# Performance work log

Measured on AMD Instinct MI355X. Metric: run time of the kernel, lower is better.

The kernel has to match this reference:

```python
import jax, jax.numpy as jnp
import numpy as np
from math import sqrt

B, L, S, H, E, D = 4, 2048, 2048, 16, 64, 64


def setup_inputs() -> dict:
    key = jax.random.key(0)
    kq, kk, kv = jax.random.split(key, 3)
    queries = jax.random.normal(kq, (B, L, H, E), dtype=jnp.float32)
    keys = jax.random.normal(kk, (B, S, H, E), dtype=jnp.float32)
    values = jax.random.normal(kv, (B, S, H, D), dtype=jnp.float32)
    # TriangularCausalMask: True above the diagonal (positions to mask out)
    attn_mask = jnp.broadcast_to(
        jnp.triu(jnp.ones((L, S), dtype=bool), k=1)[None, None], (B, 1, L, S)
    )
    return {"queries": queries, "keys": keys, "values": values, "attn_mask": attn_mask}


def reference(queries, keys, values, attn_mask):
    # B, L, H, E = queries.shape ; scale = 1/sqrt(E) (self.scale is None)
    scale = 1.0 / sqrt(queries.shape[-1])
    # scores: [B, H, L, S]
    scores = jnp.einsum("blhe,bshe->bhls", queries, keys)
    # mask_flag=True: masked_fill with -inf before scaling (scale*(-inf) = -inf)
    scores = jnp.where(attn_mask, -jnp.inf, scores)
    A = jax.nn.softmax(scale * scores, axis=-1)  # dropout p=0.0 -> identity
    V = jnp.einsum("bhls,bshd->blhd", A, values)
    return V
```

## Files before the change

### kernel.cpp

```cpp
#include <hip/hip_runtime.h>
#include <hip/hip_bf16.h>

typedef __bf16 bf16x8 __attribute__((ext_vector_type(8)));
typedef float floatx4 __attribute__((ext_vector_type(4)));
typedef unsigned int u32;

#define Bc 4
#define Lc 2048
#define Sc 2048
#define Hc 16
#define Ec 64
#define Dc 64
#define NQT (Lc/64)
#define NPAIR (NQT/2)
#define NT (Sc/64)
#define TILEB 8192
#define WSK ((size_t)Bc*Hc*NT*TILEB)
#define WSNEED (2*WSK)

__device__ __forceinline__ bf16x8 pack8f(const float* f){
  bf16x8 r;
  #pragma unroll
  for (int i=0;i<8;++i) r[i] = (__bf16)f[i];
  return r;
}

template<int CTRL>
__device__ __forceinline__ float dppf(float x){
  return __builtin_bit_cast(float,
    __builtin_amdgcn_update_dpp(0, __builtin_bit_cast(int, x), CTRL, 0xF, 0xF, true));
}
__device__ __forceinline__ float rowmax16(float x){
  x = fmaxf(x, dppf<0xB1>(x));
  x = fmaxf(x, dppf<0x4E>(x));
  x = fmaxf(x, dppf<0x141>(x));
  x = fmaxf(x, dppf<0x140>(x));
  return x;
}
__device__ __forceinline__ float rowsum16(float x){
  x += dppf<0xB1>(x);
  x += dppf<0x4E>(x);
  x += dppf<0x141>(x);
  x += dppf<0x140>(x);
  return x;
}

__device__ __forceinline__ void gload16(const void* g, void* l){
  __builtin_amdgcn_global_load_lds(
      (const __attribute__((address_space(1))) u32*)g,
      (__attribute__((address_space(3))) u32*)l, 16, 0, 0);
}

__global__ __launch_bounds__(256)
void prep(const float* __restrict__ K, const float* __restrict__ V,
          char* __restrict__ ws)
{
  const int t = blockIdx.x*256 + threadIdx.x;
  if (t < (1<<20)) {
    const int c = t & 7, r = (t>>3) & 63, tile = (t>>9) & 31, h = (t>>14) & 15, b = t>>18;
    const float* src = K + ((size_t)((b*Sc + tile*64 + r))*Hc + h)*Ec + c*8;
    float tmp[8];
    *(float4*)(tmp)   = *(const float4*)(src);
    *(float4*)(tmp+4) = *(const float4*)(src + 4);
    char* dst = ws + (size_t)((b*Hc + h)*NT + tile)*TILEB + r*128 + ((c ^ (r&7))<<4);
    *(bf16x8*)dst = pack8f(tmp);
  } else {
    const int u = t - (1<<20);
    const int d = u & 63, c = (u>>6) & 7, tile = (u>>9) & 31, h = (u>>14) & 15, b = u>>18;
    const float* src = V + ((size_t)((b*Sc + tile*64 + c*8))*Hc + h)*Dc + d;
    bf16x8 v;
    #pragma unroll
    for (int kk=0; kk<8; ++kk) v[kk] = (__bf16)src[(size_t)kk*Hc*Dc];
    char* dst = ws + WSK + (size_t)((b*Hc + h)*NT + tile)*TILEB + d*128 + ((c ^ (d&7))<<4);
    *(bf16x8*)dst = v;
  }
}

__global__ __launch_bounds__(256)
void fa_fwd(const float* __restrict__ Q, const char* __restrict__ ws,
            float* __restrict__ O)
{
  int nid = blockIdx.x;
  int bid = (nid & 7) * ((int)gridDim.x >> 3) + (nid >> 3);
  int pid = bid & (NPAIR - 1);
  int h  = (bid >> 4) & (Hc - 1);
  int b  = bid >> 8;

  int tid  = threadIdx.x;
  int w    = tid >> 6;
  int lane = tid & 63;
  int lg   = lane >> 4;
  int lr   = lane & 15;

  __shared__ __align__(16) char Kl[2][64*128];
  __shared__ __align__(16) char Vl[2][64*128];
  __shared__ __align__(16) char Pl[4][16*64*2];
  char* Pw = Pl[w];

  const char* gK = ws +        (size_t)((b*Hc + h)*NT)*TILEB;
  const char* gV = ws + WSK +  (size_t)((b*Hc + h)*NT)*TILEB;
  const int soff = w*2048 + lane*16;

  #pragma unroll 1
  for (int pass=0; pass<2; ++pass) {
    const int qt = pass ? (NQT-1-pid) : pid;

    const int qrow = qt*64 + w*16 + lr;
    const float* qp = Q + ((size_t)(b*Lc + qrow)*Hc + h)*Ec;
    bf16x8 aq[2];
    {
      float tmp[8];
      #pragma unroll
      for (int c=0; c<2; ++c) {
        *(float4*)(tmp)   = *(const float4*)(qp + c*32 + lg*8);
        *(float4*)(tmp+4) = *(const float4*)(qp + c*32 + lg*8 + 4);
        #pragma unroll
        for (int i=0;i<8;++i) tmp[i] *= 0.125f;
        aq[c] = pack8f(tmp);
      }
    }

    floatx4 o[4];
    float m[4], lsum[4];
    #pragma unroll
    for (int i=0;i<4;++i){ o[i] = (floatx4){0.f,0.f,0.f,0.f}; m[i] = -3.0e38f; lsum[i] = 0.f; }

    {
      const char* sK = gK + soff;
      const char* sV = gV + soff;
      gload16(sK,        &Kl[0][w*2048]);
      gload16(sK + 1024, &Kl[0][w*2048 + 1024]);
      gload16(sV,        &Vl[0][w*2048]);
      gload16(sV + 1024, &Vl[0][w*2048 + 1024]);
    }
    __syncthreads();

    const int nt = qt + 1;
    for (int t = 0; t < nt; ++t) {
      char* Kcur = Kl[t&1];
      char* Vcur = Vl[t&1];

      if (t+1 < nt) {
        const int nb = (t+1)&1;
        const char* sK = gK + (size_t)(t+1)*TILEB + soff;
        const char* sV = gV + (size_t)(t+1)*TILEB + soff;
        gload16(sK,        &Kl[nb][w*2048]);
        gload16(sK + 1024, &Kl[nb][w*2048 + 1024]);
        gload16(sV,        &Vl[nb][w*2048]);
        gload16(sV + 1024, &Vl[nb][w*2048 + 1024]);
      }

      floatx4 s[4];
      #pragma unroll
      for (int nf=0; nf<4; ++nf) {
        int kr = nf*16 + lr;
        unsigned xr = (kr & 7) << 4;
        const char* kp = Kcur + kr*128;
        bf16x8 b0 = *(const bf16x8*)(kp + ((lg*16)      ^ xr));
        bf16x8 b1 = *(const bf16x8*)(kp + ((64 + lg*16) ^ xr));
        floatx4 acc = (floatx4){0.f,0.f,0.f,0.f};
        acc = __builtin_amdgcn_mfma_f32_16x16x32_bf16(aq[0], b0, acc, 0, 0, 0);
        acc = __builtin_amdgcn_mfma_f32_16x16x32_bf16(aq[1], b1, acc, 0, 0, 0);
        s[nf] = acc;
      }

      if (t == qt) {
        #pragma unroll
        for (int nf=0; nf<4; ++nf)
          #pragma unroll
          for (int r=0; r<4; ++r)
            if (nf*16 + lr > w*16 + lg*4 + r) s[nf][r] = -3.0e38f;
      }

      float mx[4], rs[4], al[4];
      #pragma unroll
      for (int r=0;r<4;++r) {
        mx[r] = rowmax16(fmaxf(fmaxf(s[0][r], s[1][r]), fmaxf(s[2][r], s[3][r])));
        float mn = fmaxf(m[r], mx[r]);
        al[r] = __expf(m[r] - mn);
        m[r] = mn;
        rs[r] = 0.f;
      }
      #pragma unroll
      for (int nf=0; nf<4; ++nf)
        #pragma unroll
        for (int r=0;r<4;++r) {
          float p = __expf(s[nf][r] - m[r]);
          rs[r] += p;
          s[nf][r] = p;
        }
      #pragma unroll
      for (int r=0;r<4;++r) {
        rs[r] = rowsum16(rs[r]);
        lsum[r] = lsum[r]*al[r] + rs[r];
      }
      #pragma unroll
      for (int df=0; df<4; ++df)
        #pragma unroll
        for (int r=0;r<4;++r) o[df][r] *= al[r];

      #pragma unroll
      for (int nf=0; nf<4; ++nf)
        #pragma unroll
        for (int r=0;r<4;++r) {
          int q = lg*4 + r;
          int k = nf*16 + lr;
          *(__bf16*)(Pw + q*128 + ((k*2) ^ ((q&7)<<4))) = (__bf16)s[nf][r];
        }

      {
        unsigned xq = (lr & 7) << 4;
        const char* pp = Pw + lr*128;
        bf16x8 pa0 = *(const bf16x8*)(pp + ((lg*16)      ^ xq));
        bf16x8 pa1 = *(const bf16x8*)(pp + ((64 + lg*16) ^ xq));
        #pragma unroll
        for (int df=0; df<4; ++df) {
          int d = df*16 + lr;
          unsigned xd = (d & 7) << 4;
          const char* vp = Vcur + d*128;
          bf16x8 vb0 = *(const bf16x8*)(vp + ((lg*16)      ^ xd));
          bf16x8 vb1 = *(const bf16x8*)(vp + ((64 + lg*16) ^ xd));
          o[df] = __builtin_amdgcn_mfma_f32_16x16x32_bf16(pa0, vb0, o[df], 0, 0, 0);
          o[df] = __builtin_amdgcn_mfma_f32_16x16x32_bf16(pa1, vb1, o[df], 0, 0, 0);
        }
      }
      __syncthreads();
    }

    #pragma unroll
    for (int r=0;r<4;++r) {
      float inv = 1.0f / lsum[r];
      int qg = qt*64 + w*16 + lg*4 + r;
      float* op = O + ((size_t)(b*Lc + qg)*Hc + h)*Dc;
      #pragma unroll
      for (int df=0; df<4; ++df)
        op[df*16 + lr] = o[df][r] * inv;
    }
  }
}

#define QB 128
#define NQTB (Lc/QB)
#define NPAIRB (NQTB/2)

__global__ __launch_bounds__(256)
void fa_fwd_fb(const float* __restrict__ Q, const float* __restrict__ K,
               const float* __restrict__ V, float* __restrict__ O)
{
  int nid = blockIdx.x;
  int bid = (nid & 7) * ((int)gridDim.x >> 3) + (nid >> 3);
  int pid = bid & (NPAIRB - 1);
  int h  = (bid >> 3) & (Hc - 1);
  int b  = bid >> 7;

  int tid  = threadIdx.x;
  int w    = tid >> 6;
  int lane = tid & 63;
  int lg   = lane >> 4;
  int lr   = lane & 15;

  __shared__ __align__(16) char Kl[2][64*128];
  __shared__ __align__(16) char Vl[2][64*128];
  __shared__ __align__(16) char Pl[4][16*64*2];
  char* Pw = Pl[w];

  const int skr = tid >> 2, seg = tid & 3;
  const int sd  = tid & 63, skb = tid >> 6;
  const unsigned xk = (skr & 7) << 4;
  const unsigned xv = (sd  & 7) << 4;

  const float* Kb = K + ((size_t)(b*Sc)*Hc + h)*Ec;
  const float* Vb = V + ((size_t)(b*Sc)*Hc + h)*Dc;

  float kf[16], vf[16];

  #pragma unroll 1
  for (int pass=0; pass<2; ++pass) {
    const int qtb = pass ? (NQTB-1-pid) : pid;
    const int q0w = qtb*QB + w*32;

    bf16x8 aq[2][2];
    #pragma unroll
    for (int s2=0; s2<2; ++s2) {
      const float* qp = Q + ((size_t)(b*Lc + q0w + s2*16 + lr)*Hc + h)*Ec;
      float tmp[8];
      #pragma unroll
      for (int c=0; c<2; ++c) {
        *(float4*)(tmp)   = *(const float4*)(qp + c*32 + lg*8);
        *(float4*)(tmp+4) = *(const float4*)(qp + c*32 + lg*8 + 4);
        #pragma unroll
        for (int i=0;i<8;++i) tmp[i] *= 0.125f;
        aq[s2][c] = pack8f(tmp);
      }
    }

    floatx4 o[2][4];
    float m[2][4], lsum[2][4];
    #pragma unroll
    for (int s2=0; s2<2; ++s2)
      #pragma unroll
      for (int i=0;i<4;++i){ o[s2][i] = (floatx4){0.f,0.f,0.f,0.f}; m[s2][i] = -3.0e38f; lsum[s2][i] = 0.f; }

    {
      const float* ks = Kb + (size_t)skr*Hc*Ec + seg*16;
      *(float4*)(kf)    = *(const float4*)(ks);
      *(float4*)(kf+4)  = *(const float4*)(ks+4);
      *(float4*)(kf+8)  = *(const float4*)(ks+8);
      *(float4*)(kf+12) = *(const float4*)(ks+12);
      const float* vs = Vb + (size_t)(skb*16)*Hc*Dc + sd;
      #pragma unroll
      for (int i=0;i<16;++i) vf[i] = vs[(size_t)i*Hc*Dc];
    }

    const int nt = 2*qtb + 2;
    for (int t = 0; t < nt; ++t) {
      char* Kcur = Kl[t&1];
      char* Vcur = Vl[t&1];

      *(bf16x8*)(Kcur + skr*128 + ((seg*32)      ^ xk)) = pack8f(kf);
      *(bf16x8*)(Kcur + skr*128 + ((seg*32 + 16) ^ xk)) = pack8f(kf+8);
      *(bf16x8*)(Vcur + sd*128  + ((skb*32)      ^ xv)) = pack8f(vf);
      *(bf16x8*)(Vcur + sd*128  + ((skb*32 + 16) ^ xv)) = pack8f(vf+8);
      __syncthreads();

      if (t+1 < nt) {
        const float* ks = Kb + (size_t)((t+1)*64 + skr)*Hc*Ec + seg*16;
        *(float4*)(kf)    = *(const float4*)(ks);
        *(float4*)(kf+4)  = *(const float4*)(ks+4);
        *(float4*)(kf+8)  = *(const float4*)(ks+8);
        *(float4*)(kf+12) = *(const float4*)(ks+12);
        const float* vs = Vb + (size_t)((t+1)*64 + skb*16)*Hc*Dc + sd;
        #pragma unroll
        for (int i=0;i<16;++i) vf[i] = vs[(size_t)i*Hc*Dc];
      }

      if (t*64 <= q0w + 31) {
        const int t64 = t*64;
        const bool needmask = (t64 + 63 > q0w);

        #pragma unroll
        for (int s2=0; s2<2; ++s2) {
          floatx4 s[4];
          #pragma unroll
          for (int nf=0; nf<4; ++nf) {
            int kr = nf*16 + lr;
            unsigned xr = (kr & 7) << 4;
            const char* kp = Kcur + kr*128;
            bf16x8 b0 = *(const bf16x8*)(kp + ((lg*16)      ^ xr));
            bf16x8 b1 = *(const bf16x8*)(kp + ((64 + lg*16) ^ xr));
            floatx4 acc = (floatx4){0.f,0.f,0.f,0.f};
            acc = __builtin_amdgcn_mfma_f32_16x16x32_bf16(aq[s2][0], b0, acc, 0, 0, 0);
            acc = __builtin_amdgcn_mfma_f32_16x16x32_bf16(aq[s2][1], b1, acc, 0, 0, 0);
            s[nf] = acc;
          }

          if (needmask) {
            const int qq = q0w + s2*16 + lg*4;
            #pragma unroll
            for (int nf=0; nf<4; ++nf)
              #pragma unroll
              for (int r=0; r<4; ++r)
                if (t64 + nf*16 + lr > qq + r) s[nf][r] = -3.0e38f;
          }

          float mx[4], rs[4], al[4];
          #pragma unroll
          for (int r=0;r<4;++r) {
            mx[r] = rowmax16(fmaxf(fmaxf(s[0][r], s[1][r]), fmaxf(s[2][r], s[3][r])));
            float mn = fmaxf(m[s2][r], mx[r]);
            al[r] = __expf(m[s2][r] - mn);
            m[s2][r] = mn;
            rs[r] = 0.f;
          }
          #pragma unroll
          for (int nf=0; nf<4; ++nf)
            #pragma unroll
            for (int r=0;r<4;++r) {
              float p = __expf(s[nf][r] - m[s2][r]);
              rs[r] += p;
              s[nf][r] = p;
            }
          #pragma unroll
          for (int r=0;r<4;++r) {
            rs[r] = rowsum16(rs[r]);
            lsum[s2][r] = lsum[s2][r]*al[r] + rs[r];
          }
          #pragma unroll
          for (int df=0; df<4; ++df)
            #pragma unroll
            for (int r=0;r<4;++r) o[s2][df][r] *= al[r];

          #pragma unroll
          for (int nf=0; nf<4; ++nf)
            #pragma unroll
            for (int r=0;r<4;++r) {
              int q = lg*4 + r;
              int k = nf*16 + lr;
              *(__bf16*)(Pw + q*128 + ((k*2) ^ ((q&7)<<4))) = (__bf16)s[nf][r];
            }

          {
            unsigned xq = (lr & 7) << 4;
            const char* pp = Pw + lr*128;
            bf16x8 pa0 = *(const bf16x8*)(pp + ((lg*16)      ^ xq));
            bf16x8 pa1 = *(const bf16x8*)(pp + ((64 + lg*16) ^ xq));
            #pragma unroll
            for (int df=0; df<4; ++df) {
              int d = df*16 + lr;
              unsigned xd = (d & 7) << 4;
              const char* vp = Vcur + d*128;
              bf16x8 vb0 = *(const bf16x8*)(vp + ((lg*16)      ^ xd));
              bf16x8 vb1 = *(const bf16x8*)(vp + ((64 + lg*16) ^ xd));
              o[s2][df] = __builtin_amdgcn_mfma_f32_16x16x32_bf16(pa0, vb0, o[s2][df], 0, 0, 0);
              o[s2][df] = __builtin_amdgcn_mfma_f32_16x16x32_bf16(pa1, vb1, o[s2][df], 0, 0, 0);
            }
          }
        }
      }
      __syncthreads();
    }

    #pragma unroll
    for (int s2=0; s2<2; ++s2)
      #pragma unroll
      for (int r=0;r<4;++r) {
        float inv = 1.0f / lsum[s2][r];
        int qg = q0w + s2*16 + lg*4 + r;
        float* op = O + ((size_t)(b*Lc + qg)*Hc + h)*Dc;
        #pragma unroll
        for (int df=0; df<4; ++df)
          op[df*16 + lr] = o[s2][df][r] * inv;
      }
  }
}

extern "C" void kernel_launch(void* const* d_in, const int* in_sizes, int n_in,
                              void* d_out, int out_size, void* d_ws, size_t ws_size,
                              hipStream_t stream) {
  const float* Q = (const float*)d_in[0];
  const float* K = (const float*)d_in[1];
  const float* V = (const float*)d_in[2];
  float* O = (float*)d_out;

  if (ws_size >= WSNEED) {
    char* ws = (char*)d_ws;
    prep<<<dim3((2u<<20)/256), dim3(256), 0, stream>>>(K, V, ws);
    fa_fwd<<<dim3(Bc * Hc * NPAIR), dim3(256), 0, stream>>>(Q, ws, O);
  } else {
    fa_fwd_fb<<<dim3(Bc * Hc * NPAIRB), dim3(256), 0, stream>>>(Q, K, V, O);
  }
}
```

Before: 111.7 us.

## Use exp2 with folded log2e scale, lazy rescaling, and MFMA row sums

Folds log2(e)/sqrt(E) into the Q prescale so the softmax can use exp2f directly. The online-softmax max is only updated, and the output rescaled, when some row's max grows past a threshold; the check is wave-uniform via __any. The row-sum DPP reductions are replaced by two extra MFMAs that multiply P by a ones vector. This trims VALU and cross-lane work per tile, at the cost of two more MFMAs and a sum built from bf16-rounded P, which could slightly change numerics.

After: 122.4 us. 9.6% more time.

```diff
diff --git a/kernel.cpp b/kernel.cpp
--- a/kernel.cpp
+++ b/kernel.cpp
@@ -17,6 +17,8 @@
 #define TILEB 8192
 #define WSK ((size_t)Bc*Hc*NT*TILEB)
 #define WSNEED (2*WSK)
+#define QSC 0.18033688011112042f
+#define THR 11.5f
 
 __device__ __forceinline__ bf16x8 pack8f(const float* f){
   bf16x8 r;
@@ -101,6 +103,10 @@
   const char* gV = ws + WSK +  (size_t)((b*Hc + h)*NT)*TILEB;
   const int soff = w*2048 + lane*16;
 
+  bf16x8 ones;
+  #pragma unroll
+  for (int i=0;i<8;++i) ones[i] = (__bf16)1.0f;
+
   #pragma unroll 1
   for (int pass=0; pass<2; ++pass) {
     const int qt = pass ? (NQT-1-pid) : pid;
@@ -115,15 +121,16 @@
         *(float4*)(tmp)   = *(const float4*)(qp + c*32 + lg*8);
         *(float4*)(tmp+4) = *(const float4*)(qp + c*32 + lg*8 + 4);
         #pragma unroll
-        for (int i=0;i<8;++i) tmp[i] *= 0.125f;
+        for (int i=0;i<8;++i) tmp[i] *= QSC;
         aq[c] = pack8f(tmp);
       }
     }
 
-    floatx4 o[4];
-    float m[4], lsum[4];
-    #pragma unroll
-    for (int i=0;i<4;++i){ o[i] = (floatx4){0.f,0.f,0.f,0.f}; m[i] = -3.0e38f; lsum[i] = 0.f; }
+    floatx4 o[4], ol;
+    float m[4];
+    #pragma unroll
+    for (int i=0;i<4;++i){ o[i] = (floatx4){0.f,0.f,0.f,0.f}; m[i] = -3.0e38f; }
+    ol = (floatx4){0.f,0.f,0.f,0.f};
 
     {
       const char* sK = gK + soff;
@@ -172,32 +179,30 @@
             if (nf*16 + lr > w*16 + lg*4 + r) s[nf][r] = -3.0e38f;
       }
 
-      float mx[4], rs[4], al[4];
+      float mx[4];
+      float need = 0.f;
       #pragma unroll
       for (int r=0;r<4;++r) {
         mx[r] = rowmax16(fmaxf(fmaxf(s[0][r], s[1][r]), fmaxf(s[2][r], s[3][r])));
-        float mn = fmaxf(m[r], mx[r]);
-        al[r] = __expf(m[r] - mn);
-        m[r] = mn;
-        rs[r] = 0.f;
-      }
+        need = fmaxf(need, mx[r] - m[r]);
+      }
+      if (__any(need > THR)) {
+        #pragma unroll
+        for (int r=0;r<4;++r) {
+          float mn = fmaxf(m[r], mx[r]);
+          float al = exp2f(m[r] - mn);
+          m[r] = mn;
+          #pragma unroll
+          for (int df=0; df<4; ++df) o[df][r] *= al;
+          ol[r] *= al;
+        }
+      }
+
       #pragma unroll
       for (int nf=0; nf<4; ++nf)
         #pragma unroll
-        for (int r=0;r<4;++r) {
-          float p = __expf(s[nf][r] - m[r]);
-          rs[r] += p;
-          s[nf][r] = p;
-        }
-      #pragma unroll
-      for (int r=0;r<4;++r) {
-        rs[r] = rowsum16(rs[r]);
-        lsum[r] = lsum[r]*al[r] + rs[r];
-      }
-      #pragma unroll
-      for (int df=0; df<4; ++df)
-        #pragma unroll
-        for (int r=0;r<4;++r) o[df][r] *= al[r];
+        for (int r=0;r<4;++r)
+          s[nf][r] = exp2f(s[nf][r] - m[r]);
 
       #pragma unroll
       for (int nf=0; nf<4; ++nf)
@@ -213,6 +218,8 @@
         const char* pp = Pw + lr*128;
         bf16x8 pa0 = *(const bf16x8*)(pp + ((lg*16)      ^ xq));
         bf16x8 pa1 = *(const bf16x8*)(pp + ((64 + lg*16) ^ xq));
+        ol = __builtin_amdgcn_mfma_f32_16x16x32_bf16(pa0, ones, ol, 0, 0, 0);
+        ol = __builtin_amdgcn_mfma_f32_16x16x32_bf16(pa1, ones, ol, 0, 0, 0);
         #pragma unroll
         for (int df=0; df<4; ++df) {
           int d = df*16 + lr;
@@ -229,7 +236,7 @@
 
     #pragma unroll
     for (int r=0;r<4;++r) {
-      float inv = 1.0f / lsum[r];
+      float inv = 1.0f / ol[r];
       int qg = qt*64 + w*16 + lg*4 + r;
       float* op = O + ((size_t)(b*Lc + qg)*Hc + h)*Dc;
       #pragma unroll
```

## Use 128-row query tiles in prepped kernel and exp2 softmax with folded log2e

Applied to the files above, without the earlier changes.

The main prepped-workspace kernel now gives each wave 32 query rows (two 16-row subtiles) instead of 16, so each block covers 128 queries. Every K/V tile loaded into LDS is therefore reused by twice as many rows, and the grid is halved. The log2(e) factor is folded into the Q scaling constant so the softmax can use exp2f instead of __expf. The cost is more registers per thread for the doubled accumulators, fewer blocks in flight, and coarser causal load balance, with some waves skipping tiles that lie entirely above the diagonal.

Result: slower. 140.0 us (+25.3%).

```diff
diff --git a/kernel.cpp b/kernel.cpp
--- a/kernel.cpp
+++ b/kernel.cpp
@@ -11,12 +11,14 @@
 #define Hc 16
 #define Ec 64
 #define Dc 64
-#define NQT (Lc/64)
-#define NPAIR (NQT/2)
 #define NT (Sc/64)
 #define TILEB 8192
 #define WSK ((size_t)Bc*Hc*NT*TILEB)
 #define WSNEED (2*WSK)
+#define QSC 0.18033688011112042f
+#define QB 128
+#define NQTB (Lc/QB)
+#define NPAIRB (NQTB/2)
 
 __device__ __forceinline__ bf16x8 pack8f(const float* f){
   bf16x8 r;
@@ -82,9 +84,9 @@
 {
   int nid = blockIdx.x;
   int bid = (nid & 7) * ((int)gridDim.x >> 3) + (nid >> 3);
-  int pid = bid & (NPAIR - 1);
-  int h  = (bid >> 4) & (Hc - 1);
-  int b  = bid >> 8;
+  int pid = bid & (NPAIRB - 1);
+  int h  = (bid >> 3) & (Hc - 1);
+  int b  = bid >> 7;
 
   int tid  = threadIdx.x;
   int w    = tid >> 6;
@@ -103,27 +105,30 @@
 
   #pragma unroll 1
   for (int pass=0; pass<2; ++pass) {
-    const int qt = pass ? (NQT-1-pid) : pid;
-
-    const int qrow = qt*64 + w*16 + lr;
-    const float* qp = Q + ((size_t)(b*Lc + qrow)*Hc + h)*Ec;
-    bf16x8 aq[2];
-    {
+    const int qtb = pass ? (NQTB-1-pid) : pid;
+    const int q0w = qtb*QB + w*32;
+
+    bf16x8 aq[2][2];
+    #pragma unroll
+    for (int s2=0; s2<2; ++s2) {
+      const float* qp = Q + ((size_t)(b*Lc + q0w + s2*16 + lr)*Hc + h)*Ec;
       float tmp[8];
       #pragma unroll
       for (int c=0; c<2; ++c) {
         *(float4*)(tmp)   = *(const float4*)(qp + c*32 + lg*8);
         *(float4*)(tmp+4) = *(const float4*)(qp + c*32 + lg*8 + 4);
         #pragma unroll
-        for (int i=0;i<8;++i) tmp[i] *= 0.125f;
-        aq[c] = pack8f(tmp);
-      }
-    }
-
-    floatx4 o[4];
-    float m[4], lsum[4];
-    #pragma unroll
-    for (int i=0;i<4;++i){ o[i] = (floatx4){0.f,0.f,0.f,0.f}; m[i] = -3.0e38f; lsum[i] = 0.f; }
+        for (int i=0;i<8;++i) tmp[i] *= QSC;
+        aq[s2][c] = pack8f(tmp);
+      }
+    }
+
+    floatx4 o[2][4];
+    float m[2][4], lsum[2][4];
+    #pragma unroll
+    for (int s2=0; s2<2; ++s2)
+      #pragma unroll
+      for (int i=0;i<4;++i){ o[s2][i] = (floatx4){0.f,0.f,0.f,0.f}; m[s2][i] = -3.0e38f; lsum[s2][i] = 0.f; }
 
     {
       const char* sK = gK + soff;
@@ -135,7 +140,7 @@
     }
     __syncthreads();
 
-    const int nt = qt + 1;
+    const int nt = 2*qtb + 2;
     for (int t = 0; t < nt; ++t) {
       char* Kcur = Kl[t&1];
       char* Vcur = Vl[t&1];
@@ -148,190 +153,6 @@
         gload16(sK + 1024, &Kl[nb][w*2048 + 1024]);
         gload16(sV,        &Vl[nb][w*2048]);
         gload16(sV + 1024, &Vl[nb][w*2048 + 1024]);
-      }
-
-      floatx4 s[4];
-      #pragma unroll
-      for (int nf=0; nf<4; ++nf) {
-        int kr = nf*16 + lr;
-        unsigned xr = (kr & 7) << 4;
-        const char* kp = Kcur + kr*128;
-        bf16x8 b0 = *(const bf16x8*)(kp + ((lg*16)      ^ xr));
-        bf16x8 b1 = *(const bf16x8*)(kp + ((64 + lg*16) ^ xr));
-        floatx4 acc = (floatx4){0.f,0.f,0.f,0.f};
-        acc = __builtin_amdgcn_mfma_f32_16x16x32_bf16(aq[0], b0, acc, 0, 0, 0);
-        acc = __builtin_amdgcn_mfma_f32_16x16x32_bf16(aq[1], b1, acc, 0, 0, 0);
-        s[nf] = acc;
-      }
-
-      if (t == qt) {
-        #pragma unroll
-        for (int nf=0; nf<4; ++nf)
-          #pragma unroll
-          for (int r=0; r<4; ++r)
-            if (nf*16 + lr > w*16 + lg*4 + r) s[nf][r] = -3.0e38f;
-      }
-
-      float mx[4], rs[4], al[4];
-      #pragma unroll
-      for (int r=0;r<4;++r) {
-        mx[r] = rowmax16(fmaxf(fmaxf(s[0][r], s[1][r]), fmaxf(s[2][r], s[3][r])));
-        float mn = fmaxf(m[r], mx[r]);
-        al[r] = __expf(m[r] - mn);
-        m[r] = mn;
-        rs[r] = 0.f;
-      }
-      #pragma unroll
-      for (int nf=0; nf<4; ++nf)
-        #pragma unroll
-        for (int r=0;r<4;++r) {
-          float p = __expf(s[nf][r] - m[r]);
-          rs[r] += p;
-          s[nf][r] = p;
-        }
-      #pragma unroll
-      for (int r=0;r<4;++r) {
-        rs[r] = rowsum16(rs[r]);
-        lsum[r] = lsum[r]*al[r] + rs[r];
-      }
-      #pragma unroll
-      for (int df=0; df<4; ++df)
-        #pragma unroll
-        for (int r=0;r<4;++r) o[df][r] *= al[r];
-
-      #pragma unroll
-      for (int nf=0; nf<4; ++nf)
-        #pragma unroll
-        for (int r=0;r<4;++r) {
-          int q = lg*4 + r;
-          int k = nf*16 + lr;
-          *(__bf16*)(Pw + q*128 + ((k*2) ^ ((q&7)<<4))) = (__bf16)s[nf][r];
-        }
-
-      {
-        unsigned xq = (lr & 7) << 4;
-        const char* pp = Pw + lr*128;
-        bf16x8 pa0 = *(const bf16x8*)(pp + ((lg*16)      ^ xq));
-        bf16x8 pa1 = *(const bf16x8*)(pp + ((64 + lg*16) ^ xq));
-        #pragma unroll
-        for (int df=0; df<4; ++df) {
-          int d = df*16 + lr;
-          unsigned xd = (d & 7) << 4;
-          const char* vp = Vcur + d*128;
-          bf16x8 vb0 = *(const bf16x8*)(vp + ((lg*16)      ^ xd));
-          bf16x8 vb1 = *(const bf16x8*)(vp + ((64 + lg*16) ^ xd));
-          o[df] = __builtin_amdgcn_mfma_f32_16x16x32_bf16(pa0, vb0, o[df], 0, 0, 0);
-          o[df] = __builtin_amdgcn_mfma_f32_16x16x32_bf16(pa1, vb1, o[df], 0, 0, 0);
-        }
-      }
-      __syncthreads();
-    }
-
-    #pragma unroll
-    for (int r=0;r<4;++r) {
-      float inv = 1.0f / lsum[r];
-      int qg = qt*64 + w*16 + lg*4 + r;
-      float* op = O + ((size_t)(b*Lc + qg)*Hc + h)*Dc;
-      #pragma unroll
-      for (int df=0; df<4; ++df)
-        op[df*16 + lr] = o[df][r] * inv;
-    }
-  }
-}
-
-#define QB 128
-#define NQTB (Lc/QB)
-#define NPAIRB (NQTB/2)
-
-__global__ __launch_bounds__(256)
-void fa_fwd_fb(const float* __restrict__ Q, const float* __restrict__ K,
-               const float* __restrict__ V, float* __restrict__ O)
-{
-  int nid = blockIdx.x;
-  int bid = (nid & 7) * ((int)gridDim.x >> 3) + (nid >> 3);
-  int pid = bid & (NPAIRB - 1);
-  int h  = (bid >> 3) & (Hc - 1);
-  int b  = bid >> 7;
-
-  int tid  = threadIdx.x;
-  int w    = tid >> 6;
-  int lane = tid & 63;
-  int lg   = lane >> 4;
-  int lr   = lane & 15;
-
-  __shared__ __align__(16) char Kl[2][64*128];
-  __shared__ __align__(16) char Vl[2][64*128];
-  __shared__ __align__(16) char Pl[4][16*64*2];
-  char* Pw = Pl[w];
-
-  const int skr = tid >> 2, seg = tid & 3;
-  const int sd  = tid & 63, skb = tid >> 6;
-  const unsigned xk = (skr & 7) << 4;
-  const unsigned xv = (sd  & 7) << 4;
-
-  const float* Kb = K + ((size_t)(b*Sc)*Hc + h)*Ec;
-  const float* Vb = V + ((size_t)(b*Sc)*Hc + h)*Dc;
-
-  float kf[16], vf[16];
-
-  #pragma unroll 1
-  for (int pass=0; pass<2; ++pass) {
-    const int qtb = pass ? (NQTB-1-pid) : pid;
-    const int q0w = qtb*QB + w*32;
-
-    bf16x8 aq[2][2];
-    #pragma unroll
-    for (int s2=0; s2<2; ++s2) {
-      const float* qp = Q + ((size_t)(b*Lc + q0w + s2*16 + lr)*Hc + h)*Ec;
-      float tmp[8];
-      #pragma unroll
-      for (int c=0; c<2; ++c) {
-        *(float4*)(tmp)   = *(const float4*)(qp + c*32 + lg*8);
-        *(float4*)(tmp+4) = *(const float4*)(qp + c*32 + lg*8 + 4);
-        #pragma unroll
-        for (int i=0;i<8;++i) tmp[i] *= 0.125f;
-        aq[s2][c] = pack8f(tmp);
-      }
-    }
-
-    floatx4 o[2][4];
-    float m[2][4], lsum[2][4];
-    #pragma unroll
-    for (int s2=0; s2<2; ++s2)
-      #pragma unroll
-      for (int i=0;i<4;++i){ o[s2][i] = (floatx4){0.f,0.f,0.f,0.f}; m[s2][i] = -3.0e38f; lsum[s2][i] = 0.f; }
-
-    {
-      const float* ks = Kb + (size_t)skr*Hc*Ec + seg*16;
-      *(float4*)(kf)    = *(const float4*)(ks);
-      *(float4*)(kf+4)  = *(const float4*)(ks+4);
-      *(float4*)(kf+8)  = *(const float4*)(ks+8);
-      *(float4*)(kf+12) = *(const float4*)(ks+12);
-      const float* vs = Vb + (size_t)(skb*16)*Hc*Dc + sd;
-      #pragma unroll
-      for (int i=0;i<16;++i) vf[i] = vs[(size_t)i*Hc*Dc];
-    }
-
-    const int nt = 2*qtb + 2;
-    for (int t = 0; t < nt; ++t) {
-      char* Kcur = Kl[t&1];
-      char* Vcur = Vl[t&1];
-
-      *(bf16x8*)(Kcur + skr*128 + ((seg*32)      ^ xk)) = pack8f(kf);
-      *(bf16x8*)(Kcur + skr*128 + ((seg*32 + 16) ^ xk)) = pack8f(kf+8);
-      *(bf16x8*)(Vcur + sd*128  + ((skb*32)      ^ xv)) = pack8f(vf);
-      *(bf16x8*)(Vcur + sd*128  + ((skb*32 + 16) ^ xv)) = pack8f(vf+8);
-      __syncthreads();
-
-      if (t+1 < nt) {
-        const float* ks = Kb + (size_t)((t+1)*64 + skr)*Hc*Ec + seg*16;
-        *(float4*)(kf)    = *(const float4*)(ks);
-        *(float4*)(kf+4)  = *(const float4*)(ks+4);
-        *(float4*)(kf+8)  = *(const float4*)(ks+8);
-        *(float4*)(kf+12) = *(const float4*)(ks+12);
-        const float* vs = Vb + (size_t)((t+1)*64 + skb*16)*Hc*Dc + sd;
-        #pragma unroll
-        for (int i=0;i<16;++i) vf[i] = vs[(size_t)i*Hc*Dc];
       }
 
       if (t*64 <= q0w + 31) {
@@ -368,7 +189,7 @@
           for (int r=0;r<4;++r) {
             mx[r] = rowmax16(fmaxf(fmaxf(s[0][r], s[1][r]), fmaxf(s[2][r], s[3][r])));
             float mn = fmaxf(m[s2][r], mx[r]);
-            al[r] = __expf(m[s2][r] - mn);
+            al[r] = exp2f(m[s2][r] - mn);
             m[s2][r] = mn;
             rs[r] = 0.f;
           }
@@ -376,7 +197,7 @@
           for (int nf=0; nf<4; ++nf)
             #pragma unroll
             for (int r=0;r<4;++r) {
-              float p = __expf(s[nf][r] - m[s2][r]);
+              float p = exp2f(s[nf][r] - m[s2][r]);
               rs[r] += p;
               s[nf][r] = p;
             }
@@ -434,6 +255,197 @@
   }
 }
 
+__global__ __launch_bounds__(256)
+void fa_fwd_fb(const float* __restrict__ Q, const float* __restrict__ K,
+               const float* __restrict__ V, float* __restrict__ O)
+{
+  int nid = blockIdx.x;
+  int bid = (nid & 7) * ((int)gridDim.x >> 3) + (nid >> 3);
+  int pid = bid & (NPAIRB - 1);
+  int h  = (bid >> 3) & (Hc - 1);
+  int b  = bid >> 7;
+
+  int tid  = threadIdx.x;
+  int w    = tid >> 6;
+  int lane = tid & 63;
+  int lg   = lane >> 4;
+  int lr   = lane & 15;
+
+  __shared__ __align__(16) char Kl[2][64*128];
+  __shared__ __align__(16) char Vl[2][64*128];
+  __shared__ __align__(16) char Pl[4][16*64*2];
+  char* Pw = Pl[w];
+
+  const int skr = tid >> 2, seg = tid & 3;
+  const int sd  = tid & 63, skb = tid >> 6;
+  const unsigned xk = (skr & 7) << 4;
+  const unsigned xv = (sd  & 7) << 4;
+
+  const float* Kb = K + ((size_t)(b*Sc)*Hc + h)*Ec;
+  const float* Vb = V + ((size_t)(b*Sc)*Hc + h)*Dc;
+
+  float kf[16], vf[16];
+
+  #pragma unroll 1
+  for (int pass=0; pass<2; ++pass) {
+    const int qtb = pass ? (NQTB-1-pid) : pid;
+    const int q0w = qtb*QB + w*32;
+
+    bf16x8 aq[2][2];
+    #pragma unroll
+    for (int s2=0; s2<2; ++s2) {
+      const float* qp = Q + ((size_t)(b*Lc + q0w + s2*16 + lr)*Hc + h)*Ec;
+      float tmp[8];
+      #pragma unroll
+      for (int c=0; c<2; ++c) {
+        *(float4*)(tmp)   = *(const float4*)(qp + c*32 + lg*8);
+        *(float4*)(tmp+4) = *(const float4*)(qp + c*32 + lg*8 + 4);
+        #pragma unroll
+        for (int i=0;i<8;++i) tmp[i] *= 0.125f;
+        aq[s2][c] = pack8f(tmp);
+      }
+    }
+
+    floatx4 o[2][4];
+    float m[2][4], lsum[2][4];
+    #pragma unroll
+    for (int s2=0; s2<2; ++s2)
+      #pragma unroll
+      for (int i=0;i<4;++i){ o[s2][i] = (floatx4){0.f,0.f,0.f,0.f}; m[s2][i] = -3.0e38f; lsum[s2][i] = 0.f; }
+
+    {
+      const float* ks = Kb + (size_t)skr*Hc*Ec + seg*16;
+      *(float4*)(kf)    = *(const float4*)(ks);
+      *(float4*)(kf+4)  = *(const float4*)(ks+4);
+      *(float4*)(kf+8)  = *(const float4*)(ks+8);
+      *(float4*)(kf+12) = *(const float4*)(ks+12);
+      const float* vs = Vb + (size_t)(skb*16)*Hc*Dc + sd;
+      #pragma unroll
+      for (int i=0;i<16;++i) vf[i] = vs[(size_t)i*Hc*Dc];
+    }
+
+    const int nt = 2*qtb + 2;
+    for (int t = 0; t < nt; ++t) {
+      char* Kcur = Kl[t&1];
+      char* Vcur = Vl[t&1];
+
+      *(bf16x8*)(Kcur + skr*128 + ((seg*32)      ^ xk)) = pack8f(kf);
+      *(bf16x8*)(Kcur + skr*128 + ((seg*32 + 16) ^ xk)) = pack8f(kf+8);
+      *(bf16x8*)(Vcur + sd*128  + ((skb*32)      ^ xv)) = pack8f(vf);
+      *(bf16x8*)(Vcur + sd*128  + ((skb*32 + 16) ^ xv)) = pack8f(vf+8);
+      __syncthreads();
+
+      if (t+1 < nt) {
+        const float* ks = Kb + (size_t)((t+1)*64 + skr)*Hc*Ec + seg*16;
+        *(float4*)(kf)    = *(const float4*)(ks);
+        *(float4*)(kf+4)  = *(const float4*)(ks+4);
+        *(float4*)(kf+8)  = *(const float4*)(ks+8);
+        *(float4*)(kf+12) = *(const float4*)(ks+12);
+        const float* vs = Vb + (size_t)((t+1)*64 + skb*16)*Hc*Dc + sd;
+        #pragma unroll
+        for (int i=0;i<16;++i) vf[i] = vs[(size_t)i*Hc*Dc];
+      }
+
+      if (t*64 <= q0w + 31) {
+        const int t64 = t*64;
+        const bool needmask = (t64 + 63 > q0w);
+
+        #pragma unroll
+        for (int s2=0; s2<2; ++s2) {
+          floatx4 s[4];
+          #pragma unroll
+          for (int nf=0; nf<4; ++nf) {
+            int kr = nf*16 + lr;
+            unsigned xr = (kr & 7) << 4;
+            const char* kp = Kcur + kr*128;
+            bf16x8 b0 = *(const bf16x8*)(kp + ((lg*16)      ^ xr));
+            bf16x8 b1 = *(const bf16x8*)(kp + ((64 + lg*16) ^ xr));
+            floatx4 acc = (floatx4){0.f,0.f,0.f,0.f};
+            acc = __builtin_amdgcn_mfma_f32_16x16x32_bf16(aq[s2][0], b0, acc, 0, 0, 0);
+            acc = __builtin_amdgcn_mfma_f32_16x16x32_bf16(aq[s2][1], b1, acc, 0, 0, 0);
+            s[nf] = acc;
+          }
+
+          if (needmask) {
+            const int qq = q0w + s2*16 + lg*4;
+            #pragma unroll
+            for (int nf=0; nf<4; ++nf)
+              #pragma unroll
+              for (int r=0; r<4; ++r)
+                if (t64 + nf*16 + lr > qq + r) s[nf][r] = -3.0e38f;
+          }
+
+          float mx[4], rs[4], al[4];
+          #pragma unroll
+          for (int r=0;r<4;++r) {
+            mx[r] = rowmax16(fmaxf(fmaxf(s[0][r], s[1][r]), fmaxf(s[2][r], s[3][r])));
+            float mn = fmaxf(m[s2][r], mx[r]);
+            al[r] = __expf(m[s2][r] - mn);
+            m[s2][r] = mn;
+            rs[r] = 0.f;
+          }
+          #pragma unroll
+          for (int nf=0; nf<4; ++nf)
+            #pragma unroll
+            for (int r=0;r<4;++r) {
+              float p = __expf(s[nf][r] - m[s2][r]);
+              rs[r] += p;
+              s[nf][r] = p;
+            }
+          #pragma unroll
+          for (int r=0;r<4;++r) {
+            rs[r] = rowsum16(rs[r]);
+            lsum[s2][r] = lsum[s2][r]*al[r] + rs[r];
+          }
+          #pragma unroll
+          for (int df=0; df<4; ++df)
+            #pragma unroll
+            for (int r=0;r<4;++r) o[s2][df][r] *= al[r];
+
+          #pragma unroll
+          for (int nf=0; nf<4; ++nf)
+            #pragma unroll
+            for (int r=0;r<4;++r) {
+              int q = lg*4 + r;
+              int k = nf*16 + lr;
+              *(__bf16*)(Pw + q*128 + ((k*2) ^ ((q&7)<<4))) = (__bf16)s[nf][r];
+            }
+
+          {
+            unsigned xq = (lr & 7) << 4;
+            const char* pp = Pw + lr*128;
+            bf16x8 pa0 = *(const bf16x8*)(pp + ((lg*16)      ^ xq));
+            bf16x8 pa1 = *(const bf16x8*)(pp + ((64 + lg*16) ^ xq));
+            #pragma unroll
+            for (int df=0; df<4; ++df) {
+              int d = df*16 + lr;
+              unsigned xd = (d & 7) << 4;
+              const char* vp = Vcur + d*128;
+              bf16x8 vb0 = *(const bf16x8*)(vp + ((lg*16)      ^ xd));
+              bf16x8 vb1 = *(const bf16x8*)(vp + ((64 + lg*16) ^ xd));
+              o[s2][df] = __builtin_amdgcn_mfma_f32_16x16x32_bf16(pa0, vb0, o[s2][df], 0, 0, 0);
+              o[s2][df] = __builtin_amdgcn_mfma_f32_16x16x32_bf16(pa1, vb1, o[s2][df], 0, 0, 0);
+            }
+          }
+        }
+      }
+      __syncthreads();
+    }
+
+    #pragma unroll
+    for (int s2=0; s2<2; ++s2)
+      #pragma unroll
+      for (int r=0;r<4;++r) {
+        float inv = 1.0f / lsum[s2][r];
+        int qg = q0w + s2*16 + lg*4 + r;
+        float* op = O + ((size_t)(b*Lc + qg)*Hc + h)*Dc;
+        #pragma unroll
+        for (int df=0; df<4; ++df)
+          op[df*16 + lr] = o[s2][df][r] * inv;
+      }
+  }
+}
+
 extern "C" void kernel_launch(void* const* d_in, const int* in_sizes, int n_in,
                               void* d_out, int out_size, void* d_ws, size_t ws_size,
                               hipStream_t stream) {
@@ -445,7 +457,7 @@
   if (ws_size >= WSNEED) {
     char* ws = (char*)d_ws;
     prep<<<dim3((2u<<20)/256), dim3(256), 0, stream>>>(K, V, ws);
-    fa_fwd<<<dim3(Bc * Hc * NPAIR), dim3(256), 0, stream>>>(Q, ws, O);
+    fa_fwd<<<dim3(Bc * Hc * NPAIRB), dim3(256), 0, stream>>>(Q, ws, O);
   } else {
     fa_fwd_fb<<<dim3(Bc * Hc * NPAIRB), dim3(256), 0, stream>>>(Q, K, V, O);
   }
```

## Process paired query tiles in one KV sweep and use exp2 softmax

Applied to the files above, without the earlier changes.

The two paired query tiles (pid and its mirror) are now computed together in a single loop over KV tiles instead of two sequential passes. Each K/V tile is loaded into shared memory once and reused by both strips, which removes the duplicate loads and the extra pipeline ramp-up for the shorter tile. Q is also prescaled by log2(e)/sqrt(E), so the softmax uses exp2f instead of __expf. The cost is doubled accumulator and state registers per thread, which may reduce occupancy, and both strips share the one per-warp P buffer in sequence.

Result: slower. 138.7 us (+24.2%).

```diff
diff --git a/kernel.cpp b/kernel.cpp
--- a/kernel.cpp
+++ b/kernel.cpp
@@ -17,6 +17,7 @@
 #define TILEB 8192
 #define WSK ((size_t)Bc*Hc*NT*TILEB)
 #define WSNEED (2*WSK)
+#define QSC 0.18033688011112042f
 
 __device__ __forceinline__ bf16x8 pack8f(const float* f){
   bf16x8 r;
@@ -76,6 +77,80 @@
   }
 }
 
+#define STRIP_COMPUTE(AQ, OO, MM, LS, QT)                                        \
+  {                                                                              \
+    floatx4 s[4];                                                                \
+    _Pragma("unroll")                                                            \
+    for (int nf=0; nf<4; ++nf) {                                                 \
+      int kr = nf*16 + lr;                                                       \
+      unsigned xr = (kr & 7) << 4;                                               \
+      const char* kp = Kcur + kr*128;                                            \
+      bf16x8 b0 = *(const bf16x8*)(kp + ((lg*16)      ^ xr));                    \
+      bf16x8 b1 = *(const bf16x8*)(kp + ((64 + lg*16) ^ xr));                    \
+      floatx4 acc = (floatx4){0.f,0.f,0.f,0.f};                                  \
+      acc = __builtin_amdgcn_mfma_f32_16x16x32_bf16(AQ[0], b0, acc, 0, 0, 0);    \
+      acc = __builtin_amdgcn_mfma_f32_16x16x32_bf16(AQ[1], b1, acc, 0, 0, 0);    \
+      s[nf] = acc;                                                               \
+    }                                                                            \
+    if (t == (QT)) {                                                             \
+      _Pragma("unroll")                                                          \
+      for (int nf=0; nf<4; ++nf)                                                 \
+        _Pragma("unroll")                                                        \
+        for (int r=0; r<4; ++r)                                                  \
+          if (nf*16 + lr > w*16 + lg*4 + r) s[nf][r] = -3.0e38f;                 \
+    }                                                                            \
+    float mx[4], rs[4], al[4];                                                   \
+    _Pragma("unroll")                                                            \
+    for (int r=0;r<4;++r) {                                                      \
+      mx[r] = rowmax16(fmaxf(fmaxf(s[0][r], s[1][r]), fmaxf(s[2][r], s[3][r]))); \
+      float mn = fmaxf(MM[r], mx[r]);                                            \
+      al[r] = exp2f(MM[r] - mn);                                                 \
+      MM[r] = mn;                                                                \
+      rs[r] = 0.f;                                                               \
+    }                                                                            \
+    _Pragma("unroll")                                                            \
+    for (int nf=0; nf<4; ++nf)                                                   \
+      _Pragma("unroll")                                                          \
+      for (int r=0;r<4;++r) {                                                    \
+        float p = exp2f(s[nf][r] - MM[r]);                                       \
+        rs[r] += p;                                                              \
+        s[nf][r] = p;                                                            \
+      }                                                                          \
+    _Pragma("unroll")                                                            \
+    for (int r=0;r<4;++r) {                                                      \
+      rs[r] = rowsum16(rs[r]);                                                   \
+      LS[r] = LS[r]*al[r] + rs[r];                                               \
+    }                                                                            \
+    _Pragma("unroll")                                                            \
+    for (int df=0; df<4; ++df)                                                   \
+      _Pragma("unroll")                                                          \
+      for (int r=0;r<4;++r) OO[df][r] *= al[r];                                  \
+    _Pragma("unroll")                                                            \
+    for (int nf=0; nf<4; ++nf)                                                   \
+      _Pragma("unroll")                                                          \
+      for (int r=0;r<4;++r) {                                                    \
+        int q = lg*4 + r;                                                        \
+        int k = nf*16 + lr;                                                      \
+        *(__bf16*)(Pw + q*128 + ((k*2) ^ ((q&7)<<4))) = (__bf16)s[nf][r];        \
+      }                                                                          \
+    {                                                                            \
+      unsigned xq = (lr & 7) << 4;                                               \
+      const char* pp = Pw + lr*128;                                              \
+      bf16x8 pa0 = *(const bf16x8*)(pp + ((lg*16)      ^ xq));                   \
+      bf16x8 pa1 = *(const bf16x8*)(pp + ((64 + lg*16) ^ xq));                   \
+      _Pragma("unroll")                                                          \
+      for (int df=0; df<4; ++df) {                                               \
+        int d = df*16 + lr;                                                      \
+        unsigned xd = (d & 7) << 4;                                              \
+        const char* vp = Vcur + d*128;                                           \
+        bf16x8 vb0 = *(const bf16x8*)(vp + ((lg*16)      ^ xd));                 \
+        bf16x8 vb1 = *(const bf16x8*)(vp + ((64 + lg*16) ^ xd));                 \
+        OO[df] = __builtin_amdgcn_mfma_f32_16x16x32_bf16(pa0, vb0, OO[df], 0,0,0);\
+        OO[df] = __builtin_amdgcn_mfma_f32_16x16x32_bf16(pa1, vb1, OO[df], 0,0,0);\
+      }                                                                          \
+    }                                                                            \
+  }
+
 __global__ __launch_bounds__(256)
 void fa_fwd(const float* __restrict__ Q, const char* __restrict__ ws,
             float* __restrict__ O)
@@ -101,140 +176,82 @@
   const char* gV = ws + WSK +  (size_t)((b*Hc + h)*NT)*TILEB;
   const int soff = w*2048 + lane*16;
 
-  #pragma unroll 1
-  for (int pass=0; pass<2; ++pass) {
-    const int qt = pass ? (NQT-1-pid) : pid;
-
-    const int qrow = qt*64 + w*16 + lr;
-    const float* qp = Q + ((size_t)(b*Lc + qrow)*Hc + h)*Ec;
-    bf16x8 aq[2];
-    {
-      float tmp[8];
-      #pragma unroll
-      for (int c=0; c<2; ++c) {
-        *(float4*)(tmp)   = *(const float4*)(qp + c*32 + lg*8);
-        *(float4*)(tmp+4) = *(const float4*)(qp + c*32 + lg*8 + 4);
-        #pragma unroll
-        for (int i=0;i<8;++i) tmp[i] *= 0.125f;
-        aq[c] = pack8f(tmp);
-      }
-    }
-
-    floatx4 o[4];
-    float m[4], lsum[4];
-    #pragma unroll
-    for (int i=0;i<4;++i){ o[i] = (floatx4){0.f,0.f,0.f,0.f}; m[i] = -3.0e38f; lsum[i] = 0.f; }
-
-    {
-      const char* sK = gK + soff;
-      const char* sV = gV + soff;
-      gload16(sK,        &Kl[0][w*2048]);
-      gload16(sK + 1024, &Kl[0][w*2048 + 1024]);
-      gload16(sV,        &Vl[0][w*2048]);
-      gload16(sV + 1024, &Vl[0][w*2048 + 1024]);
-    }
+  const int qtA = pid;
+  const int qtB = NQT - 1 - pid;
+
+  bf16x8 aqA[2], aqB[2];
+  {
+    const float* qpA = Q + ((size_t)(b*Lc + qtA*64 + w*16 + lr)*Hc + h)*Ec;
+    const float* qpB = Q + ((size_t)(b*Lc + qtB*64 + w*16 + lr)*Hc + h)*Ec;
+    float tmp[8];
+    #pragma unroll
+    for (int c=0; c<2; ++c) {
+      *(float4*)(tmp)   = *(const float4*)(qpA + c*32 + lg*8);
+      *(float4*)(tmp+4) = *(const float4*)(qpA + c*32 + lg*8 + 4);
+      #pragma unroll
+      for (int i=0;i<8;++i) tmp[i] *= QSC;
+      aqA[c] = pack8f(tmp);
+      *(float4*)(tmp)   = *(const float4*)(qpB + c*32 + lg*8);
+      *(float4*)(tmp+4) = *(const float4*)(qpB + c*32 + lg*8 + 4);
+      #pragma unroll
+      for (int i=0;i<8;++i) tmp[i] *= QSC;
+      aqB[c] = pack8f(tmp);
+    }
+  }
+
+  floatx4 oA[4], oB[4];
+  float mA[4], lsA[4], mB[4], lsB[4];
+  #pragma unroll
+  for (int i=0;i<4;++i){
+    oA[i] = (floatx4){0.f,0.f,0.f,0.f}; mA[i] = -3.0e38f; lsA[i] = 0.f;
+    oB[i] = (floatx4){0.f,0.f,0.f,0.f}; mB[i] = -3.0e38f; lsB[i] = 0.f;
+  }
+
+  {
+    const char* sK = gK + soff;
+    const char* sV = gV + soff;
+    gload16(sK,        &Kl[0][w*2048]);
+    gload16(sK + 1024, &Kl[0][w*2048 + 1024]);
+    gload16(sV,        &Vl[0][w*2048]);
+    gload16(sV + 1024, &Vl[0][w*2048 + 1024]);
+  }
+  __syncthreads();
+
+  const int nt = qtB + 1;
+  for (int t = 0; t < nt; ++t) {
+    char* Kcur = Kl[t&1];
+    char* Vcur = Vl[t&1];
+
+    if (t+1 < nt) {
+      const int nb = (t+1)&1;
+      const char* sK = gK + (size_t)(t+1)*TILEB + soff;
+      const char* sV = gV + (size_t)(t+1)*TILEB + soff;
+      gload16(sK,        &Kl[nb][w*2048]);
+      gload16(sK + 1024, &Kl[nb][w*2048 + 1024]);
+      gload16(sV,        &Vl[nb][w*2048]);
+      gload16(sV + 1024, &Vl[nb][w*2048 + 1024]);
+    }
+
+    STRIP_COMPUTE(aqB, oB, mB, lsB, qtB)
+
+    if (t <= qtA) {
+      STRIP_COMPUTE(aqA, oA, mA, lsA, qtA)
+    }
+
     __syncthreads();
-
-    const int nt = qt + 1;
-    for (int t = 0; t < nt; ++t) {
-      char* Kcur = Kl[t&1];
-      char* Vcur = Vl[t&1];
-
-      if (t+1 < nt) {
-        const int nb = (t+1)&1;
-        const char* sK = gK + (size_t)(t+1)*TILEB + soff;
-        const char* sV = gV + (size_t)(t+1)*TILEB + soff;
-        gload16(sK,        &Kl[nb][w*2048]);
-        gload16(sK + 1024, &Kl[nb][w*2048 + 1024]);
-        gload16(sV,        &Vl[nb][w*2048]);
-        gload16(sV + 1024, &Vl[nb][w*2048 + 1024]);
-      }
-
-      floatx4 s[4];
-      #pragma unroll
-      for (int nf=0; nf<4; ++nf) {
-        int kr = nf*16 + lr;
-        unsigned xr = (kr & 7) << 4;
-        const char* kp = Kcur + kr*128;
-        bf16x8 b0 = *(const bf16x8*)(kp + ((lg*16)      ^ xr));
-        bf16x8 b1 = *(const bf16x8*)(kp + ((64 + lg*16) ^ xr));
-        floatx4 acc = (floatx4){0.f,0.f,0.f,0.f};
-        acc = __builtin_amdgcn_mfma_f32_16x16x32_bf16(aq[0], b0, acc, 0, 0, 0);
-        acc = __builtin_amdgcn_mfma_f32_16x16x32_bf16(aq[1], b1, acc, 0, 0, 0);
-        s[nf] = acc;
-      }
-
-      if (t == qt) {
-        #pragma unroll
-        for (int nf=0; nf<4; ++nf)
-          #pragma unroll
-          for (int r=0; r<4; ++r)
-            if (nf*16 + lr > w*16 + lg*4 + r) s[nf][r] = -3.0e38f;
-      }
-
-      float mx[4], rs[4], al[4];
-      #pragma unroll
-      for (int r=0;r<4;++r) {
-        mx[r] = rowmax16(fmaxf(fmaxf(s[0][r], s[1][r]), fmaxf(s[2][r], s[3][r])));
-        float mn = fmaxf(m[r], mx[r]);
-        al[r] = __expf(m[r] - mn);
-        m[r] = mn;
-        rs[r] = 0.f;
-      }
-      #pragma unroll
-      for (int nf=0; nf<4; ++nf)
-        #pragma unroll
-        for (int r=0;r<4;++r) {
-          float p = __expf(s[nf][r] - m[r]);
-          rs[r] += p;
-          s[nf][r] = p;
-        }
-      #pragma unroll
-      for (int r=0;r<4;++r) {
-        rs[r] = rowsum16(rs[r]);
-        lsum[r] = lsum[r]*al[r] + rs[r];
-      }
-      #pragma unroll
-      for (int df=0; df<4; ++df)
-        #pragma unroll
-        for (int r=0;r<4;++r) o[df][r] *= al[r];
-
-      #pragma unroll
-      for (int nf=0; nf<4; ++nf)
-        #pragma unroll
-        for (int r=0;r<4;++r) {
-          int q = lg*4 + r;
-          int k = nf*16 + lr;
-          *(__bf16*)(Pw + q*128 + ((k*2) ^ ((q&7)<<4))) = (__bf16)s[nf][r];
-        }
-
-      {
-        unsigned xq = (lr & 7) << 4;
-        const char* pp = Pw + lr*128;
-        bf16x8 pa0 = *(const bf16x8*)(pp + ((lg*16)      ^ xq));
-        bf16x8 pa1 = *(const bf16x8*)(pp + ((64 + lg*16) ^ xq));
-        #pragma unroll
-        for (int df=0; df<4; ++df) {
-          int d = df*16 + lr;
-          unsigned xd = (d & 7) << 4;
-          const char* vp = Vcur + d*128;
-          bf16x8 vb0 = *(const bf16x8*)(vp + ((lg*16)      ^ xd));
-          bf16x8 vb1 = *(const bf16x8*)(vp + ((64 + lg*16) ^ xd));
-          o[df] = __builtin_amdgcn_mfma_f32_16x16x32_bf16(pa0, vb0, o[df], 0, 0, 0);
-          o[df] = __builtin_amdgcn_mfma_f32_16x16x32_bf16(pa1, vb1, o[df], 0, 0, 0);
-        }
-      }
-      __syncthreads();
-    }
-
-    #pragma unroll
-    for (int r=0;r<4;++r) {
-      float inv = 1.0f / lsum[r];
-      int qg = qt*64 + w*16 + lg*4 + r;
-      float* op = O + ((size_t)(b*Lc + qg)*Hc + h)*Dc;
-      #pragma unroll
-      for (int df=0; df<4; ++df)
-        op[df*16 + lr] = o[df][r] * inv;
+  }
+
+  #pragma unroll
+  for (int r=0;r<4;++r) {
+    float invA = 1.0f / lsA[r];
+    float invB = 1.0f / lsB[r];
+    int qr = w*16 + lg*4 + r;
+    float* opA = O + ((size_t)(b*Lc + qtA*64 + qr)*Hc + h)*Dc;
+    float* opB = O + ((size_t)(b*Lc + qtB*64 + qr)*Hc + h)*Dc;
+    #pragma unroll
+    for (int df=0; df<4; ++df) {
+      opA[df*16 + lr] = oA[df][r] * invA;
+      opB[df*16 + lr] = oB[df][r] * invB;
     }
   }
 }
```
